# Optimization experiments

Hardware: AMD Instinct MI355X
Metric: run time of the kernel (lower is better)

Reference implementation:

```python
import jax, jax.numpy as jnp
import numpy as np

B, CH, XL, YL = 512, 1, 64, 64
H = 64                       # num_heads
D = CH * XL * YL             # 4096
F = D // H                   # feature_dim = 64 (== H, required by the mask multiply)


def setup_inputs() -> dict:
    key = jax.random.key(0)
    k1, k2, k3, k4, k5 = jax.random.split(key, 5)
    scale = 1.0 / np.sqrt(D)  # roughly kaiming-ish init for square linears
    return {
        "x": jax.random.normal(k1, (B, CH, XL, YL), dtype=jnp.float32),
        "interface_map": jax.random.uniform(k2, (B, CH, XL, YL), dtype=jnp.float32),
        "Wq": jax.random.normal(k3, (D, D), dtype=jnp.float32) * scale,
        "Wk": jax.random.normal(k4, (D, D), dtype=jnp.float32) * scale,
        "Wv": jax.random.normal(k5, (D, D), dtype=jnp.float32) * scale,
    }


def reference(x, interface_map, Wq, Wk, Wv):
    b = x.shape[0]
    xf = x.reshape(b, D)
    # nn.Linear(bias=False): y = x @ W.T
    q = (xf @ Wq.T).reshape(b, H, F)
    k = (xf @ Wk.T).reshape(b, H, F)
    v = (xf @ Wv.T).reshape(b, H, F)
    inv_sqrt_f = jnp.float32(1.0 / np.sqrt(F))
    qk_t = jnp.einsum("bhf,bgf->bhg", q, k) * inv_sqrt_f           # (B, H, H)
    qk_t = qk_t * interface_map.reshape(b, H, F)                   # multiplicative mask (F == H)
    attention_weights = jax.nn.softmax(qk_t, axis=-1)
    weighted_values = jnp.einsum("bhg,bgf->bhf", attention_weights, v)  # (B, H, F)
    combined = jnp.swapaxes(weighted_values, 1, 2).reshape(b, CH, XL, YL)
    output = x * combined
    return output, attention_weights
```

## Files before the change

kernel.cpp:

```cpp
#include <hip/hip_runtime.h>
#include <cstdint>
#include <cstddef>

typedef __attribute__((ext_vector_type(8))) short short8;
typedef __attribute__((ext_vector_type(4))) float f32x4;

#define NB 512
#define DD 4096
#define NP 12288

__device__ __forceinline__ unsigned short f2bf(float f) {
    unsigned u = __float_as_uint(f);
    u += 0x7fffu + ((u >> 16) & 1u);
    return (unsigned short)(u >> 16);
}
__device__ __forceinline__ unsigned pack2bf(float a, float b) {
    return (unsigned)f2bf(a) | ((unsigned)f2bf(b) << 16);
}

__device__ __forceinline__ void gload_lds16(const void* g, void* l) {
    __builtin_amdgcn_global_load_lds((const __attribute__((address_space(1))) void*)g,
                                     (__attribute__((address_space(3))) void*)l, 16, 0, 0);
}

__global__ __launch_bounds__(256) void cvt_bf16_kernel(const float* __restrict__ src,
                                                       unsigned short* __restrict__ dst,
                                                       int n8) {
    int i = blockIdx.x * 256 + threadIdx.x;
    if (i >= n8) return;
    const float4* s = (const float4*)src + (size_t)i * 2;
    float4 a = s[0], b = s[1];
    uint4 r;
    r.x = pack2bf(a.x, a.y);
    r.y = pack2bf(a.z, a.w);
    r.z = pack2bf(b.x, b.y);
    r.w = pack2bf(b.z, b.w);
    ((uint4*)dst)[i] = r;
}

template<int KS>
__global__ __launch_bounds__(256, 3) void gemm_qkv_kernel(
    const unsigned short* __restrict__ xb,
    const float* __restrict__ w0, const float* __restrict__ w1, const float* __restrict__ w2,
    float* __restrict__ part)
{
    constexpr int KLEN = DD / KS;
    constexpr int NIT = KLEN / 32;

    const int nt = blockIdx.x;
    const int mt = blockIdx.y;
    const int kz = blockIdx.z;

    const float* W = (nt < 32) ? w0 : ((nt < 64) ? w1 : w2);
    const int ntl = nt & 31;
    const float* Wbase = W + (size_t)(ntl * 128) * DD + kz * KLEN;
    const unsigned short* Abase = xb + (size_t)(mt * 128) * DD + kz * KLEN;
    float* C = part + (size_t)kz * NB * NP;

    __shared__ unsigned short As[2][128 * 32];
    __shared__ unsigned short Bs[128 * 32];

    const int t = threadIdx.x;
    const int l = t & 63;
    const int wv = t >> 6;
    const int wr = wv >> 1, wc = wv & 1;

    f32x4 acc[4][4];
    #pragma unroll
    for (int i = 0; i < 4; ++i)
        #pragma unroll
        for (int j = 0; j < 4; ++j)
            acc[i][j] = (f32x4){0.f, 0.f, 0.f, 0.f};

    const int arow0 = (t >> 2);
    const int acol  = (((t & 3) ^ ((t >> 3) & 3)) * 8);
    const int brow = t >> 1, bh = t & 1;
    const float* wrow = Wbase + (size_t)brow * DD + bh * 16;
    const int bws = (t >> 2) & 3;
    char* bw0 = (char*)(&Bs[0]) + brow * 64 + (((2 * bh) ^ bws) * 16);
    char* bw1 = (char*)(&Bs[0]) + brow * 64 + (((2 * bh + 1) ^ bws) * 16);
    const int cx = ((l >> 4) ^ ((l >> 1) & 3));

    float4 breg[4];

    #define LOADB(kt)  { _Pragma("unroll") for (int j = 0; j < 4; ++j) \
                           breg[j] = *(const float4*)(wrow + (kt) * 32 + j * 4); }
    #define STAGEA(kt, buf) { _Pragma("unroll") for (int i = 0; i < 2; ++i) \
                           gload_lds16(Abase + (size_t)(i * 64 + arow0) * DD + (kt) * 32 + acol, \
                                       (char*)(&As[buf][0]) + i * 4096 + wv * 1024); }
    #define WRITEB()   { uint4 p0, p1; \
                         p0.x = pack2bf(breg[0].x, breg[0].y); p0.y = pack2bf(breg[0].z, breg[0].w); \
                         p0.z = pack2bf(breg[1].x, breg[1].y); p0.w = pack2bf(breg[1].z, breg[1].w); \
                         p1.x = pack2bf(breg[2].x, breg[2].y); p1.y = pack2bf(breg[2].z, breg[2].w); \
                         p1.z = pack2bf(breg[3].x, breg[3].y); p1.w = pack2bf(breg[3].z, breg[3].w); \
                         *(uint4*)bw0 = p0; *(uint4*)bw1 = p1; }

    LOADB(0);
    STAGEA(0, 0);
    WRITEB();
    __syncthreads();

    for (int kt = 0; kt < NIT; ++kt) {
        const int cur = kt & 1;
        if (kt + 1 < NIT) {
            STAGEA(kt + 1, cur ^ 1);
            LOADB(kt + 1);
        }
        short8 af[4], bfr[4];
        #pragma unroll
        for (int fi = 0; fi < 4; ++fi) {
            int row = wr * 64 + fi * 16 + (l & 15);
            af[fi] = *(const short8*)((const char*)(&As[cur][0]) + row * 64 + cx * 16);
        }
        #pragma unroll
        for (int fj = 0; fj < 4; ++fj) {
            int row = wc * 64 + fj * 16 + (l & 15);
            bfr[fj] = *(const short8*)((const char*)(&Bs[0]) + row * 64 + cx * 16);
        }
        #pragma unroll
        for (int fi = 0; fi < 4; ++fi)
            #pragma unroll
            for (int fj = 0; fj < 4; ++fj)
                acc[fi][fj] = __builtin_amdgcn_mfma_f32_16x16x32_bf16(af[fi], bfr[fj], acc[fi][fj], 0, 0, 0);

        __syncthreads();
        if (kt + 1 < NIT) {
            WRITEB();
        }
        __syncthreads();
    }

    #pragma unroll
    for (int fi = 0; fi < 4; ++fi) {
        int rbase = mt * 128 + wr * 64 + fi * 16 + (l >> 4) * 4;
        #pragma unroll
        for (int fj = 0; fj < 4; ++fj) {
            int col = nt * 128 + wc * 64 + fj * 16 + (l & 15);
            #pragma unroll
            for (int r = 0; r < 4; ++r)
                C[(size_t)(rbase + r) * NP + col] = acc[fi][fj][r];
        }
    }
    #undef LOADB
    #undef STAGEA
    #undef WRITEB
}

template<int KS>
__global__ __launch_bounds__(256) void attn_kernel(
    const float* __restrict__ part,
    const float* __restrict__ x,
    const float* __restrict__ imap,
    float* __restrict__ dout)
{
    const int b = blockIdx.x;
    const int t = threadIdx.x;
    const int l = t & 63;
    const int wv = t >> 6;

    __shared__ float sq[64 * 68];
    __shared__ float sk[64 * 68];
    __shared__ float sv[64 * 68];

    const float* base0 = part + (size_t)b * NP;
    const float* base1 = part + (size_t)NB * NP + (size_t)b * NP;

    #pragma unroll
    for (int i = 0; i < 4; ++i) {
        int f4 = i * 256 + t;
        int r = f4 >> 4, c = (f4 & 15) * 4;
        float4 q4 = *(const float4*)(base0 + (size_t)f4 * 4);
        float4 k4 = *(const float4*)(base0 + DD + (size_t)f4 * 4);
        float4 v4 = *(const float4*)(base0 + 2 * DD + (size_t)f4 * 4);
        if (KS == 2) {
            float4 a4 = *(const float4*)(base1 + (size_t)f4 * 4);
            float4 b4 = *(const float4*)(base1 + DD + (size_t)f4 * 4);
            float4 c4 = *(const float4*)(base1 + 2 * DD + (size_t)f4 * 4);
            q4.x += a4.x; q4.y += a4.y; q4.z += a4.z; q4.w += a4.w;
            k4.x += b4.x; k4.y += b4.y; k4.z += b4.z; k4.w += b4.w;
            v4.x += c4.x; v4.y += c4.y; v4.z += c4.z; v4.w += c4.w;
        }
        *(float4*)(&sq[r * 68 + c]) = q4;
        *(float4*)(&sk[r * 68 + c]) = k4;
        *(float4*)(&sv[r * 68 + c]) = v4;
    }
    __syncthreads();

    float accs[16];
    #pragma unroll
    for (int i = 0; i < 16; ++i) accs[i] = 0.f;
    #pragma unroll 4
    for (int f4 = 0; f4 < 16; ++f4) {
        float4 kvv = *(const float4*)(&sk[l * 68 + f4 * 4]);
        #pragma unroll
        for (int i = 0; i < 16; ++i) {
            int h = i * 4 + wv;
            float4 qv = *(const float4*)(&sq[h * 68 + f4 * 4]);
            accs[i] = fmaf(qv.x, kvv.x, fmaf(qv.y, kvv.y, fmaf(qv.z, kvv.z, fmaf(qv.w, kvv.w, accs[i]))));
        }
    }
    __syncthreads();
    #pragma unroll
    for (int i = 0; i < 16; ++i) {
        int h = i * 4 + wv;
        float m = imap[(size_t)b * DD + h * 64 + l];
        sk[h * 65 + l] = accs[i] * 0.125f * m;
    }
    __syncthreads();

    {
        int h = t >> 2, j = t & 3;
        float e[16];
        float mx = -3.0e38f;
        #pragma unroll
        for (int q2 = 0; q2 < 16; ++q2) {
            e[q2] = sk[h * 65 + j * 16 + q2];
            mx = fmaxf(mx, e[q2]);
        }
        mx = fmaxf(mx, __shfl_xor(mx, 1));
        mx = fmaxf(mx, __shfl_xor(mx, 2));
        float s = 0.f;
        #pragma unroll
        for (int q2 = 0; q2 < 16; ++q2) { e[q2] = __expf(e[q2] - mx); s += e[q2]; }
        s += __shfl_xor(s, 1);
        s += __shfl_xor(s, 2);
        float invs = 1.0f / s;
        float* aw = dout + (size_t)NB * DD + (size_t)b * DD + h * 64 + j * 16;
        #pragma unroll
        for (int q2 = 0; q2 < 16; q2 += 4) {
            float4 w4 = {e[q2] * invs, e[q2 + 1] * invs, e[q2 + 2] * invs, e[q2 + 3] * invs};
            *(float4*)(aw + q2) = w4;
            sk[h * 65 + j * 16 + q2 + 0] = w4.x;
            sk[h * 65 + j * 16 + q2 + 1] = w4.y;
            sk[h * 65 + j * 16 + q2 + 2] = w4.z;
            sk[h * 65 + j * 16 + q2 + 3] = w4.w;
        }
    }
    __syncthreads();

    float pacc[16];
    #pragma unroll
    for (int i = 0; i < 16; ++i) pacc[i] = 0.f;
    #pragma unroll 4
    for (int g = 0; g < 64; ++g) {
        float p = sk[l * 65 + g];
        const float4* vr = (const float4*)(&sv[g * 68 + wv * 16]);
        float4 v0 = vr[0], v1 = vr[1], v2 = vr[2], v3 = vr[3];
        pacc[0]  = fmaf(p, v0.x, pacc[0]);
        pacc[1]  = fmaf(p, v0.y, pacc[1]);
        pacc[2]  = fmaf(p, v0.z, pacc[2]);
        pacc[3]  = fmaf(p, v0.w, pacc[3]);
        pacc[4]  = fmaf(p, v1.x, pacc[4]);
        pacc[5]  = fmaf(p, v1.y, pacc[5]);
        pacc[6]  = fmaf(p, v1.z, pacc[6]);
        pacc[7]  = fmaf(p, v1.w, pacc[7]);
        pacc[8]  = fmaf(p, v2.x, pacc[8]);
        pacc[9]  = fmaf(p, v2.y, pacc[9]);
        pacc[10] = fmaf(p, v2.z, pacc[10]);
        pacc[11] = fmaf(p, v2.w, pacc[11]);
        pacc[12] = fmaf(p, v3.x, pacc[12]);
        pacc[13] = fmaf(p, v3.y, pacc[13]);
        pacc[14] = fmaf(p, v3.z, pacc[14]);
        pacc[15] = fmaf(p, v3.w, pacc[15]);
    }
    const size_t ob = (size_t)b * DD + (size_t)(wv * 16) * 64 + l;
    #pragma unroll
    for (int ii = 0; ii < 16; ++ii) {
        size_t o = ob + (size_t)ii * 64;
        dout[o] = x[o] * pacc[ii];
    }
}

extern "C" void kernel_launch(void* const* d_in, const int* in_sizes, int n_in,
                              void* d_out, int out_size, void* d_ws, size_t ws_size,
                              hipStream_t stream) {
    const float* x  = (const float*)d_in[0];
    const float* im = (const float*)d_in[1];
    const float* Wq = (const float*)d_in[2];
    const float* Wk = (const float*)d_in[3];
    const float* Wv = (const float*)d_in[4];
    float* out = (float*)d_out;

    unsigned short* xb = (unsigned short*)d_ws;
    float* part = (float*)((char*)d_ws + (size_t)NB * DD * 2);

    const size_t need2 = (size_t)NB * DD * 2 + 2ull * NB * NP * 4;
    const int KS = (ws_size >= need2) ? 2 : 1;

    cvt_bf16_kernel<<<dim3((NB * DD / 8 + 255) / 256), dim3(256), 0, stream>>>(x, xb, NB * DD / 8);

    if (KS == 2) {
        gemm_qkv_kernel<2><<<dim3(96, 4, 2), dim3(256), 0, stream>>>(xb, Wq, Wk, Wv, part);
        attn_kernel<2><<<dim3(NB), dim3(256), 0, stream>>>(part, x, im, out);
    } else {
        gemm_qkv_kernel<1><<<dim3(96, 4, 1), dim3(256), 0, stream>>>(xb, Wq, Wk, Wv, part);
        attn_kernel<1><<<dim3(NB), dim3(256), 0, stream>>>(part, x, im, out);
    }
}
```

Before: 144.4 us.

## Double-buffer B tile, remap blocks across XCDs, use hardware bf16 pack

The QKV GEMM now keeps two LDS buffers for the weight tile and two register sets, prefetching weights two iterations ahead. This removes one of the two barriers per k-step and hides global load latency. The grid is flattened and block IDs are remapped so that neighbouring tiles land on the same XCD, which should improve L2 reuse of the weight and activation tiles. Software round-to-nearest bf16 conversion is replaced with the v_cvt_pk_bf16_f32 instruction. In exchange, the kernel uses more LDS and registers, which could lower occupancy.

```diff
diff --git a/kernel.cpp b/kernel.cpp
--- a/kernel.cpp
+++ b/kernel.cpp
@@ -9,13 +9,10 @@
 #define DD 4096
 #define NP 12288
 
-__device__ __forceinline__ unsigned short f2bf(float f) {
-    unsigned u = __float_as_uint(f);
-    u += 0x7fffu + ((u >> 16) & 1u);
-    return (unsigned short)(u >> 16);
-}
-__device__ __forceinline__ unsigned pack2bf(float a, float b) {
-    return (unsigned)f2bf(a) | ((unsigned)f2bf(b) << 16);
+__device__ __forceinline__ unsigned pk2(float a, float b) {
+    unsigned r;
+    asm("v_cvt_pk_bf16_f32 %0, %1, %2" : "=v"(r) : "v"(a), "v"(b));
+    return r;
 }
 
 __device__ __forceinline__ void gload_lds16(const void* g, void* l) {
@@ -31,10 +28,10 @@
     const float4* s = (const float4*)src + (size_t)i * 2;
     float4 a = s[0], b = s[1];
     uint4 r;
-    r.x = pack2bf(a.x, a.y);
-    r.y = pack2bf(a.z, a.w);
-    r.z = pack2bf(b.x, b.y);
-    r.w = pack2bf(b.z, b.w);
+    r.x = pk2(a.x, a.y);
+    r.y = pk2(a.z, a.w);
+    r.z = pk2(b.x, b.y);
+    r.w = pk2(b.z, b.w);
     ((uint4*)dst)[i] = r;
 }
 
@@ -46,10 +43,15 @@
 {
     constexpr int KLEN = DD / KS;
     constexpr int NIT = KLEN / 32;
-
-    const int nt = blockIdx.x;
-    const int mt = blockIdx.y;
-    const int kz = blockIdx.z;
+    constexpr int NWG = 96 * 4 * KS;
+    constexpr int CPX = NWG / 8;
+
+    const int bid = blockIdx.x;
+    const int orig = (bid & 7) * CPX + (bid >> 3);
+    const int nt = orig / (4 * KS);
+    const int rest = orig - nt * (4 * KS);
+    const int mt = rest / KS;
+    const int kz = rest - mt * KS;
 
     const float* W = (nt < 32) ? w0 : ((nt < 64) ? w1 : w2);
     const int ntl = nt & 31;
@@ -58,7 +60,7 @@
     float* C = part + (size_t)kz * NB * NP;
 
     __shared__ unsigned short As[2][128 * 32];
-    __shared__ unsigned short Bs[128 * 32];
+    __shared__ unsigned short Bs[2][128 * 32];
 
     const int t = threadIdx.x;
     const int l = t & 63;
@@ -77,58 +79,58 @@
     const int brow = t >> 1, bh = t & 1;
     const float* wrow = Wbase + (size_t)brow * DD + bh * 16;
     const int bws = (t >> 2) & 3;
-    char* bw0 = (char*)(&Bs[0]) + brow * 64 + (((2 * bh) ^ bws) * 16);
-    char* bw1 = (char*)(&Bs[0]) + brow * 64 + (((2 * bh + 1) ^ bws) * 16);
+    char* const bw0 = (char*)(&Bs[0][0]) + brow * 64 + (((2 * bh) ^ bws) * 16);
+    char* const bw1 = (char*)(&Bs[0][0]) + brow * 64 + (((2 * bh + 1) ^ bws) * 16);
     const int cx = ((l >> 4) ^ ((l >> 1) & 3));
 
-    float4 breg[4];
-
-    #define LOADB(kt)  { _Pragma("unroll") for (int j = 0; j < 4; ++j) \
-                           breg[j] = *(const float4*)(wrow + (kt) * 32 + j * 4); }
+    float4 bregA[4], bregB[4];
+
+    #define LOADB(br, kt)  { _Pragma("unroll") for (int j = 0; j < 4; ++j) \
+                               br[j] = *(const float4*)(wrow + (kt) * 32 + j * 4); }
     #define STAGEA(kt, buf) { _Pragma("unroll") for (int i = 0; i < 2; ++i) \
-                           gload_lds16(Abase + (size_t)(i * 64 + arow0) * DD + (kt) * 32 + acol, \
-                                       (char*)(&As[buf][0]) + i * 4096 + wv * 1024); }
-    #define WRITEB()   { uint4 p0, p1; \
-                         p0.x = pack2bf(breg[0].x, breg[0].y); p0.y = pack2bf(breg[0].z, breg[0].w); \
-                         p0.z = pack2bf(breg[1].x, breg[1].y); p0.w = pack2bf(breg[1].z, breg[1].w); \
-                         p1.x = pack2bf(breg[2].x, breg[2].y); p1.y = pack2bf(breg[2].z, breg[2].w); \
-                         p1.z = pack2bf(breg[3].x, breg[3].y); p1.w = pack2bf(breg[3].z, breg[3].w); \
-                         *(uint4*)bw0 = p0; *(uint4*)bw1 = p1; }
-
-    LOADB(0);
+                               gload_lds16(Abase + (size_t)(i * 64 + arow0) * DD + (kt) * 32 + acol, \
+                                           (char*)(&As[buf][0]) + i * 4096 + wv * 1024); }
+    #define WRITEB(br, buf) { uint4 q0, q1; \
+                              q0.x = pk2(br[0].x, br[0].y); q0.y = pk2(br[0].z, br[0].w); \
+                              q0.z = pk2(br[1].x, br[1].y); q0.w = pk2(br[1].z, br[1].w); \
+                              q1.x = pk2(br[2].x, br[2].y); q1.y = pk2(br[2].z, br[2].w); \
+                              q1.z = pk2(br[3].x, br[3].y); q1.w = pk2(br[3].z, br[3].w); \
+                              *(uint4*)(bw0 + (buf) * 8192) = q0; \
+                              *(uint4*)(bw1 + (buf) * 8192) = q1; }
+
+    LOADB(bregA, 0);
     STAGEA(0, 0);
-    WRITEB();
-    __syncthreads();
-
-    for (int kt = 0; kt < NIT; ++kt) {
-        const int cur = kt & 1;
-        if (kt + 1 < NIT) {
-            STAGEA(kt + 1, cur ^ 1);
-            LOADB(kt + 1);
-        }
-        short8 af[4], bfr[4];
-        #pragma unroll
-        for (int fi = 0; fi < 4; ++fi) {
-            int row = wr * 64 + fi * 16 + (l & 15);
-            af[fi] = *(const short8*)((const char*)(&As[cur][0]) + row * 64 + cx * 16);
-        }
-        #pragma unroll
-        for (int fj = 0; fj < 4; ++fj) {
-            int row = wc * 64 + fj * 16 + (l & 15);
-            bfr[fj] = *(const short8*)((const char*)(&Bs[0]) + row * 64 + cx * 16);
-        }
-        #pragma unroll
-        for (int fi = 0; fi < 4; ++fi)
-            #pragma unroll
-            for (int fj = 0; fj < 4; ++fj)
-                acc[fi][fj] = __builtin_amdgcn_mfma_f32_16x16x32_bf16(af[fi], bfr[fj], acc[fi][fj], 0, 0, 0);
-
-        __syncthreads();
-        if (kt + 1 < NIT) {
-            WRITEB();
-        }
-        __syncthreads();
-    }
+    WRITEB(bregA, 0);
+    LOADB(bregB, 1);
+    __syncthreads();
+
+    #define ITER(cur, nxt, bwr, bld, kt) { \
+        if ((kt) + 1 < NIT) STAGEA((kt) + 1, nxt); \
+        if ((kt) + 2 < NIT) LOADB(bld, (kt) + 2); \
+        short8 af[4], bfr[4]; \
+        _Pragma("unroll") for (int fi = 0; fi < 4; ++fi) { \
+            int row = wr * 64 + fi * 16 + (l & 15); \
+            af[fi] = *(const short8*)((const char*)(&As[cur][0]) + row * 64 + cx * 16); \
+        } \
+        _Pragma("unroll") for (int fj = 0; fj < 4; ++fj) { \
+            int row = wc * 64 + fj * 16 + (l & 15); \
+            bfr[fj] = *(const short8*)((const char*)(&Bs[cur][0]) + row * 64 + cx * 16); \
+        } \
+        _Pragma("unroll") for (int fi = 0; fi < 4; ++fi) \
+            _Pragma("unroll") for (int fj = 0; fj < 4; ++fj) \
+                acc[fi][fj] = __builtin_amdgcn_mfma_f32_16x16x32_bf16(af[fi], bfr[fj], acc[fi][fj], 0, 0, 0); \
+        if ((kt) + 1 < NIT) WRITEB(bwr, nxt); \
+        __syncthreads(); \
+    }
+
+    for (int kt = 0; kt < NIT; kt += 2) {
+        ITER(0, 1, bregB, bregA, kt);
+        ITER(1, 0, bregA, bregB, kt + 1);
+    }
+    #undef ITER
+    #undef LOADB
+    #undef STAGEA
+    #undef WRITEB
 
     #pragma unroll
     for (int fi = 0; fi < 4; ++fi) {
@@ -141,9 +143,6 @@
                 C[(size_t)(rbase + r) * NP + col] = acc[fi][fj][r];
         }
     }
-    #undef LOADB
-    #undef STAGEA
-    #undef WRITEB
 }
 
 template<int KS>
@@ -290,10 +289,10 @@
     cvt_bf16_kernel<<<dim3((NB * DD / 8 + 255) / 256), dim3(256), 0, stream>>>(x, xb, NB * DD / 8);
 
     if (KS == 2) {
-        gemm_qkv_kernel<2><<<dim3(96, 4, 2), dim3(256), 0, stream>>>(xb, Wq, Wk, Wv, part);
+        gemm_qkv_kernel<2><<<dim3(96 * 4 * 2), dim3(256), 0, stream>>>(xb, Wq, Wk, Wv, part);
         attn_kernel<2><<<dim3(NB), dim3(256), 0, stream>>>(part, x, im, out);
     } else {
-        gemm_qkv_kernel<1><<<dim3(96, 4, 1), dim3(256), 0, stream>>>(xb, Wq, Wk, Wv, part);
+        gemm_qkv_kernel<1><<<dim3(96 * 4 * 1), dim3(256), 0, stream>>>(xb, Wq, Wk, Wv, part);
         attn_kernel<1><<<dim3(NB), dim3(256), 0, stream>>>(part, x, im, out);
     }
 }
```

After: 141.7 us. About the same (-1.8%).
